# Kernel tuning notes

Hardware: AMD Instinct MI355X
Metric: run time of the kernel (lower is better)

Reference implementation:

```python
import jax, jax.numpy as jnp
import numpy as np

LMAX = 6
F_IN = 512      # sphere_fdim
F_HID = 8       # f_hidden
N_PTS = 192     # s2 healpix grid points (projector & feature-sphere kernel)
N_SO3GRID = 4000  # SO3Activation grid (resolution=10, ~20x10x20)
N_CONVGRID = 192  # so3_near_identity_grid (8 alpha x 3 beta x 8 gamma)
S2_DIM = (LMAX + 1) ** 2                            # 49
SO3_DIM = sum((2 * l + 1) ** 2 for l in range(LMAX + 1))  # 455
B = 128
C_ENC = 2048
H = W = 7


def setup_inputs() -> dict:
    key = jax.random.key(0)
    ks = jax.random.split(key, 11)
    return {
        "fmap": jax.random.normal(ks[0], (B, C_ENC, H, W), jnp.float32),
        "conv_w": jax.random.normal(ks[1], (F_IN, C_ENC), jnp.float32) / np.sqrt(C_ENC).astype(np.float32),
        "conv_b": jnp.zeros((F_IN,), jnp.float32),
        "proj_w": jax.random.uniform(ks[2], (H, W, N_PTS), jnp.float32) / (H * W),
        "proj_Y": jax.random.normal(ks[3], (N_PTS, S2_DIM), jnp.float32),
        "fs_w": jax.random.normal(ks[4], (F_IN, F_HID, N_PTS), jnp.float32),
        "fs_Y": jax.random.normal(ks[5], (N_PTS, S2_DIM), jnp.float32),
        "act_to": jax.random.normal(ks[6], (SO3_DIM, N_SO3GRID), jnp.float32) / np.sqrt(SO3_DIM).astype(np.float32),
        "act_from": jax.random.normal(ks[7], (N_SO3GRID, SO3_DIM), jnp.float32) / np.float32(N_SO3GRID),
        "so3_w": jax.random.normal(ks[8], (F_HID, 1, N_CONVGRID), jnp.float32),
        "so3_D": jax.random.normal(ks[9], (N_CONVGRID, SO3_DIM), jnp.float32),
    }


def _s2_to_so3_linear(x, psi, f_in):
    # e3nn o3.Linear(s2_irreps -> so3_irreps, internal_weights=False).
    # x: (B, f_in, S2_DIM) with per-l blocks of size 2l+1 (mul=1).
    # psi: (f_in, f_out, S2_DIM). Per l: outer product of input irrep with
    # weight irrep -> (2l+1)x(2l+1) Wigner block; path norm 1/sqrt(f_in*mul_in).
    outs = []
    for l in range(LMAX + 1):
        s, e = l * l, (l + 1) ** 2
        xl = x[:, :, s:e]          # (B, f_in, 2l+1)
        wl = psi[:, :, s:e]        # (f_in, f_out, 2l+1)
        ol = jnp.einsum('bfm,fgu->bgum', xl, wl) / np.sqrt(f_in).astype(np.float32)
        outs.append(ol.reshape(ol.shape[0], ol.shape[1], -1))
    return jnp.concatenate(outs, axis=-1)   # (B, f_out, SO3_DIM)


def _so3_to_so3_linear(x, psi, f_in):
    # e3nn o3.Linear(so3_irreps -> so3_irreps, internal_weights=False).
    # x: (B, f_in, SO3_DIM), per-l block (mul=2l+1, dim=2l+1) flattened [u, m].
    # psi: (f_in, f_out, SO3_DIM), per-l block (u_in, u_out).
    outs = []
    off = 0
    for l in range(LMAX + 1):
        d = 2 * l + 1
        xl = x[:, :, off:off + d * d].reshape(x.shape[0], f_in, d, d)
        wl = psi[:, :, off:off + d * d].reshape(f_in, psi.shape[1], d, d)
        ol = jnp.einsum('bfum,fguv->bgvm', xl, wl) / np.sqrt(f_in * d).astype(np.float32)
        outs.append(ol.reshape(ol.shape[0], ol.shape[1], -1))
        off += d * d
    return jnp.concatenate(outs, axis=-1)


def reference(fmap, conv_w, conv_b, proj_w, proj_Y, fs_w, fs_Y, act_to, act_from, so3_w, so3_D):
    # --- SpatialS2Projector: 1x1 conv, orthographic-grid weighting, S2 FT ---
    x = jnp.einsum('bchw,fc->bfhw', fmap, conv_w) + conv_b[None, :, None, None]
    x = jnp.einsum('bfhw,hwn->bfn', x, proj_w)                   # (B, 512, N_PTS)
    x = jnp.einsum('bfn,ni->bfi', x, proj_Y) / np.sqrt(N_PTS).astype(np.float32)  # (B, 512, 49)
    # --- feature sphere -> external weight for o3.Linear (S2 conv theorem) ---
    psi = jnp.einsum('fgn,ni->fgi', fs_w, fs_Y) / np.sqrt(N_PTS).astype(np.float32)  # (512, 8, 49)
    x = _s2_to_so3_linear(x, psi, F_IN)                          # (B, 8, 455)
    # --- SO3Activation: synthesize signal on SO3 grid, relu, analyze back ---
    g = jax.nn.relu(jnp.einsum('bfi,in->bfn', x, act_to))        # (B, 8, N_SO3GRID)
    x = jnp.einsum('bfn,ni->bfi', g, act_from)                   # (B, 8, 455)
    # --- SO3Convolution over near-identity grid ---
    psi2 = jnp.einsum('fgn,ni->fgi', so3_w, so3_D) / np.sqrt(N_CONVGRID).astype(np.float32)  # (8, 1, 455)
    x = _so3_to_so3_linear(x, psi2, F_HID)                       # (B, 1, 455)
    return x
```

## Files before the change

kernel.cpp:

```cpp
#include <hip/hip_runtime.h>
#include <hip/hip_bf16.h>

#define NB    128
#define CENC  2048
#define FIN   512
#define FHID  8
#define S2D   49
#define SO3D  455
#define HW    49

typedef unsigned short ushort_t;
typedef __bf16 bf16x8 __attribute__((ext_vector_type(8)));
typedef float  f32x4  __attribute__((ext_vector_type(4)));

#define GLD16(gp, lp) __builtin_amdgcn_global_load_lds( \
    (__attribute__((address_space(1))) const unsigned int*)(gp), \
    (__attribute__((address_space(3))) unsigned int*)(lp), 16, 0, 0)

__device__ __forceinline__ int soff(int l) { return l*(4*l*l-1)/3; }

__device__ __forceinline__ ushort_t f2bf(float x) {
  __hip_bfloat16 h = __float2bfloat16(x);
  return *reinterpret_cast<ushort_t*>(&h);
}
__device__ __forceinline__ float bf2f(ushort_t u) {
  __hip_bfloat16 h = *reinterpret_cast<__hip_bfloat16*>(&u);
  return __bfloat162float(h);
}


__device__ __forceinline__ void dev_gemm_nn(float* smem,
    const float* __restrict__ A, const float* __restrict__ B, float* __restrict__ C,
    int M, int N, int K, int lda, int ldb, int ldc, float alpha, int bx, int by,
    int cmode, ushort_t* __restrict__ psiTout)
{
  float* As = smem;
  float* Bs = smem + 32*68;
  const int tid = threadIdx.x;
  const int tx = tid & 15, ty = tid >> 4;
  const int n0 = bx * 64, m0 = by * 64;
  float acc[4][4] = {};
  for (int k0 = 0; k0 < K; k0 += 32) {
    {
      const int kk = tid & 31, mmB = tid >> 5;
      #pragma unroll
      for (int j = 0; j < 8; ++j) {
        const int mm = mmB + 8*j;
        const int m = m0 + mm, k = k0 + kk;
        As[kk*68 + mm] = (m < M && k < K) ? A[(size_t)m*lda + k] : 0.f;
      }
    }
    {
      const int nn = tid & 63, kkB = tid >> 6;
      #pragma unroll
      for (int j = 0; j < 8; ++j) {
        const int kk = kkB + 4*j;
        const int n = n0 + nn, k = k0 + kk;
        Bs[kk*68 + nn] = (n < N && k < K) ? B[(size_t)k*ldb + n] : 0.f;
      }
    }
    __syncthreads();
    #pragma unroll
    for (int kk = 0; kk < 32; ++kk) {
      const float4 a4 = *(const float4*)&As[kk*68 + ty*4];
      const float4 b4 = *(const float4*)&Bs[kk*68 + tx*4];
      const float av[4] = {a4.x,a4.y,a4.z,a4.w};
      const float bv[4] = {b4.x,b4.y,b4.z,b4.w};
      #pragma unroll
      for (int i = 0; i < 4; ++i)
        #pragma unroll
        for (int j = 0; j < 4; ++j)
          acc[i][j] = fmaf(av[i], bv[j], acc[i][j]);
    }
    __syncthreads();
  }
  if (cmode == 1) {
    #pragma unroll
    for (int i = 0; i < 4; ++i) {
      const int m = m0 + ty*4 + i;
      const int f = m >> 3, g = m & 7;
      #pragma unroll
      for (int j = 0; j < 4; ++j) {
        const int n = tx*4 + j;
        psiTout[(size_t)(g*64 + n)*512 + f] = (n < 49) ? f2bf(acc[i][j]*alpha) : (ushort_t)0;
      }
    }
    return;
  }
  #pragma unroll
  for (int i = 0; i < 4; ++i) {
    const int m = m0 + ty*4 + i;
    if (m >= M) continue;
    #pragma unroll
    for (int j = 0; j < 4; ++j) {
      const int n = n0 + tx*4 + j;
      if (n >= N) continue;
      C[(size_t)m*ldc + n] = acc[i][j] * alpha;
    }
  }
}

__device__ __forceinline__ void dev_transpose_cvt64(float* smem,
    const float* __restrict__ in, int R, int C,
    ushort_t* __restrict__ out, int Rp, int Cp, int bx, int by)
{
  float (*t)[65] = (float(*)[65])smem;
  const int c0 = bx*64, r0 = by*64;
  const int tid = threadIdx.x;
  const int cl = tid & 63, rlB = tid >> 6;
  #pragma unroll
  for (int p = 0; p < 16; ++p) {
    const int rl = rlB + p*4;
    const int r = r0 + rl, c = c0 + cl;
    t[rl][cl] = (r < R && c < C) ? in[(size_t)r*C + c] : 0.f;
  }
  __syncthreads();
  #pragma unroll
  for (int p = 0; p < 4; ++p) {
    const int c = p*16 + (tid >> 4);
    const int r4 = (tid & 15) * 4;
    unsigned int lo = (unsigned int)f2bf(t[r4+0][c]) | ((unsigned int)f2bf(t[r4+1][c]) << 16);
    unsigned int hi = (unsigned int)f2bf(t[r4+2][c]) | ((unsigned int)f2bf(t[r4+3][c]) << 16);
    *(uint2*)&out[(size_t)(c0 + c)*Rp + r0 + r4] = make_uint2(lo, hi);
  }
}

__device__ __forceinline__ void dev_transpose_fmap(float* smem,
    const float* __restrict__ fmap, ushort_t* __restrict__ out, int cc, int b)
{
  float* Fs = smem;
  const int tid = threadIdx.x;
  const int c0 = cc*64;
  const float* fsrc = fmap + ((size_t)b*CENC + c0)*HW;
  for (int idx = tid; idx < 784; idx += 256)
    *(float4*)&Fs[idx*4] = *(const float4*)&fsrc[idx*4];
  __syncthreads();
  for (int idx = tid; idx < 784; idx += 256) {
    const int h = idx >> 4, c4 = (idx & 15) * 4;
    unsigned int lo = (unsigned int)f2bf(Fs[(c4+0)*49 + h]) | ((unsigned int)f2bf(Fs[(c4+1)*49 + h]) << 16);
    unsigned int hi = (unsigned int)f2bf(Fs[(c4+2)*49 + h]) | ((unsigned int)f2bf(Fs[(c4+3)*49 + h]) << 16);
    *(uint2*)&out[(size_t)(b*49 + h)*CENC + c0 + c4] = make_uint2(lo, hi);
  }
}

__device__ __forceinline__ void dev_sumP(float* smem,
    const float* __restrict__ proj_w, const float* __restrict__ proj_Y,
    float* __restrict__ sumP)
{
  float* colsum = smem;
  const int tid = threadIdx.x;
  if (tid < 192) {
    float s = 0.f;
    for (int h = 0; h < 49; ++h) s += proj_w[h*192 + tid];
    colsum[tid] = s;
  }
  __syncthreads();
  if (tid < 64) {
    float s = 0.f;
    if (tid < 49) for (int k = 0; k < 192; ++k) s += colsum[k] * proj_Y[k*49 + tid];
    sumP[tid] = (tid < 49) ? s * 0.07216878364870323f : 0.f;
  }
}

__global__ __launch_bounds__(256) void prep_all(
    const float* __restrict__ fmap, const float* __restrict__ conv_w,
    const float* __restrict__ proj_w, const float* __restrict__ proj_Y,
    const float* __restrict__ fs_w, const float* __restrict__ fs_Y,
    const float* __restrict__ act_to, const float* __restrict__ act_from,
    const float* __restrict__ so3_w, const float* __restrict__ so3_D,
    float* __restrict__ wP, float* __restrict__ wSumP, float* __restrict__ wPsi2,
    ushort_t* __restrict__ psiT,
    ushort_t* __restrict__ actToT, ushort_t* __restrict__ actFromT,
    ushort_t* __restrict__ cwT, ushort_t* __restrict__ fmapT)
{
  __shared__ float smem[4352];
  const int blk = blockIdx.x;
  const float is192 = 0.07216878364870323f;
  if (blk < 1) {
    dev_gemm_nn(smem, proj_w, proj_Y, wP, 49,49,192, 192,49,49, is192, 0, 0, 0, nullptr);
  } else if (blk < 9) {
    dev_gemm_nn(smem, so3_w, so3_D, wPsi2, 8,455,192, 192,455,455, is192, blk-1, 0, 0, nullptr);
  } else if (blk < 73) {
    dev_gemm_nn(smem, fs_w, fs_Y, nullptr, 4096,49,192, 192,49,0, is192, 0, blk-9, 1, psiT);
  } else if (blk < 585) {
    const int t = blk-73;   dev_transpose_cvt64(smem, act_to, 455, 4000, actToT, 512, 4096, t & 63, t >> 6);
  } else if (blk < 1097) {
    const int t = blk-585;  dev_transpose_cvt64(smem, act_from, 4000, 455, actFromT, 4096, 512, t & 7, t >> 3);
  } else if (blk < 1353) {
    const int t = blk-1097; dev_transpose_cvt64(smem, conv_w, 512, 2048, cwT, 512, 2048, t & 31, t >> 5);
  } else if (blk < 5449) {
    const int t = blk-1353; dev_transpose_fmap(smem, fmap, fmapT, t & 31, t >> 5);
  } else {
    dev_sumP(smem, proj_w, proj_Y, wSumP);
  }
}

__global__ __launch_bounds__(256) void gemm_w2t(
    const ushort_t* __restrict__ A, const ushort_t* __restrict__ B,
    const float* __restrict__ conv_b,
    ushort_t* __restrict__ Cb, float* __restrict__ bpsi)
{
  __shared__ ushort_t Alds[64*64];
  __shared__ ushort_t Blds[128*64];
  __shared__ float bred[256];
  const int tid = threadIdx.x;
  const int wv = tid >> 6, ln = tid & 63;
  const int col = ln & 15, quad = ln >> 4;
  const int m0 = blockIdx.y * 64, n0 = blockIdx.x * 128;
  const int lda = 512, ldb = 512, ldc = 2048, K = 512;
  const bool doB = (blockIdx.x == 0);
  const int br = tid & 63, bp = tid >> 6;

  const int rl = ln >> 3;
  const int gsw = (ln & 7) ^ rl;
  const ushort_t* aP[2]; const ushort_t* bP[4];
  ushort_t* aL[2]; ushort_t* bL[4];
  #pragma unroll
  for (int r = 0; r < 2; ++r) {
    const int R = wv*16 + r*8;
    aP[r] = A + (size_t)(m0 + R + rl)*lda + gsw*8;
    aL[r] = &Alds[R*64];
  }
  #pragma unroll
  for (int r = 0; r < 4; ++r) {
    const int R = wv*32 + r*8;
    bP[r] = B + (size_t)(n0 + R + rl)*ldb + gsw*8;
    bL[r] = &Blds[R*64];
  }

  f32x4 acc[4][2];
  #pragma unroll
  for (int i = 0; i < 4; ++i)
    #pragma unroll
    for (int j = 0; j < 2; ++j)
      acc[i][j] = (f32x4){0.f,0.f,0.f,0.f};
  float bacc = 0.f;

  for (int k0 = 0; k0 < K; k0 += 64) {
    #pragma unroll
    for (int r = 0; r < 2; ++r) { GLD16(aP[r], aL[r]); aP[r] += 64; }
    #pragma unroll
    for (int r = 0; r < 4; ++r) { GLD16(bP[r], bL[r]); bP[r] += 64; }
    __syncthreads();
    #pragma unroll
    for (int ks = 0; ks < 2; ++ks) {
      bf16x8 af[4], bfr[2];
      #pragma unroll
      for (int i = 0; i < 4; ++i) {
        const int row = i*16 + col;
        af[i] = *(bf16x8*)&Alds[row*64 + (((ks*4 + quad) ^ (row & 7)) << 3)];
      }
      #pragma unroll
      for (int j = 0; j < 2; ++j) {
        const int row = wv*32 + j*16 + col;
        bfr[j] = *(bf16x8*)&Blds[row*64 + (((ks*4 + quad) ^ (row & 7)) << 3)];
      }
      #pragma unroll
      for (int i = 0; i < 4; ++i)
        #pragma unroll
        for (int j = 0; j < 2; ++j)
          acc[i][j] = __builtin_amdgcn_mfma_f32_16x16x32_bf16(af[i], bfr[j], acc[i][j], 0, 0, 0);
    }
    if (doB) {
      #pragma unroll
      for (int qq = 0; qq < 2; ++qq) {
        const int q = bp*2 + qq;
        const int lo = (q ^ (br & 7)) << 3;
        #pragma unroll
        for (int e = 0; e < 8; ++e)
          bacc = fmaf(conv_b[k0 + q*8 + e], bf2f(Alds[br*64 + lo + e]), bacc);
      }
    }
    __syncthreads();
  }

  #pragma unroll
  for (int i = 0; i < 4; ++i) {
    const int mBase = m0 + i*16 + quad*4;
    #pragma unroll
    for (int j = 0; j < 2; ++j) {
      const int n = n0 + wv*32 + j*16 + col;
      #pragma unroll
      for (int r = 0; r < 4; ++r)
        Cb[(size_t)(mBase+r)*ldc + n] = f2bf(acc[i][j][r]);
    }
  }
  if (doB) {
    bred[bp*64 + br] = bacc;
    __syncthreads();
    if (tid < 64)
      bpsi[m0 + tid] = bred[tid] + bred[64+tid] + bred[128+tid] + bred[192+tid];
  }
}

__global__ __launch_bounds__(512) void gemm8w_nt(
    const ushort_t* __restrict__ A, const ushort_t* __restrict__ B, void* __restrict__ Cv,
    int M, int N, int K, int lda, int ldb, int ldc,
    int mode, int kPartLen)
{
  __shared__ ushort_t Alds[128*64];
  __shared__ ushort_t Blds[128*64];
  const int tid = threadIdx.x;
  const int wv = tid >> 6, ln = tid & 63;
  const int col = ln & 15, quad = ln >> 4;
  const int wr = wv >> 2, wc = wv & 3;
  const int m0 = blockIdx.y * 128, n0 = blockIdx.x * 128;
  int kStart = 0, kEnd = K;
  float*    C  = (float*)Cv;
  ushort_t* Cb = (ushort_t*)Cv;
  if (mode == 2) {
    kStart = blockIdx.z * kPartLen;
    kEnd = min(K, kStart + kPartLen);
    C += (size_t)blockIdx.z * (size_t)M * (size_t)ldc;
  }

  const int rl = ln >> 3;
  const int gsw = (ln & 7) ^ rl;
  const ushort_t* aP[2]; const ushort_t* bP[2];
  ushort_t* aL[2]; ushort_t* bL[2];
  #pragma unroll
  for (int r = 0; r < 2; ++r) {
    const int R = wv*16 + r*8;
    aP[r] = A + (size_t)(m0 + R + rl)*lda + kStart + gsw*8;
    aL[r] = &Alds[R*64];
    bP[r] = B + (size_t)(n0 + R + rl)*ldb + kStart + gsw*8;
    bL[r] = &Blds[R*64];
  }

  f32x4 acc[4][2];
  #pragma unroll
  for (int i = 0; i < 4; ++i)
    #pragma unroll
    for (int j = 0; j < 2; ++j)
      acc[i][j] = (f32x4){0.f,0.f,0.f,0.f};

  for (int k0 = kStart; k0 < kEnd; k0 += 64) {
    #pragma unroll
    for (int r = 0; r < 2; ++r) { GLD16(aP[r], aL[r]); aP[r] += 64; }
    #pragma unroll
    for (int r = 0; r < 2; ++r) { GLD16(bP[r], bL[r]); bP[r] += 64; }
    __syncthreads();
    #pragma unroll
    for (int ks = 0; ks < 2; ++ks) {
      bf16x8 af[4], bfr[2];
      #pragma unroll
      for (int i = 0; i < 4; ++i) {
        const int row = wr*64 + i*16 + col;
        af[i] = *(bf16x8*)&Alds[row*64 + (((ks*4 + quad) ^ (row & 7)) << 3)];
      }
      #pragma unroll
      for (int j = 0; j < 2; ++j) {
        const int row = wc*32 + j*16 + col;
        bfr[j] = *(bf16x8*)&Blds[row*64 + (((ks*4 + quad) ^ (row & 7)) << 3)];
      }
      #pragma unroll
      for (int i = 0; i < 4; ++i)
        #pragma unroll
        for (int j = 0; j < 2; ++j)
          acc[i][j] = __builtin_amdgcn_mfma_f32_16x16x32_bf16(af[i], bfr[j], acc[i][j], 0, 0, 0);
    }
    __syncthreads();
  }

  #pragma unroll
  for (int i = 0; i < 4; ++i) {
    const int mBase = m0 + wr*64 + i*16 + quad*4;
    #pragma unroll
    for (int j = 0; j < 2; ++j) {
      const int n = n0 + wc*32 + j*16 + col;
      if (mode == 1) {
        #pragma unroll
        for (int r = 0; r < 4; ++r)
          Cb[(size_t)(mBase+r)*ldc + n] = f2bf(fmaxf(acc[i][j][r], 0.f));
      } else {
        #pragma unroll
        for (int r = 0; r < 4; ++r)
          C[(size_t)(mBase+r)*ldc + n] = acc[i][j][r];
      }
    }
  }
}

__global__ __launch_bounds__(256) void gather_y(
    const float* __restrict__ T, const float* __restrict__ P,
    const float* __restrict__ sumP, const float* __restrict__ bpsi,
    ushort_t* __restrict__ y)
{
  __shared__ float Tg[49*64];
  __shared__ float Pl[49*49];
  __shared__ float sPl[49];
  __shared__ float bps[64];
  const int tid = threadIdx.x;
  const int g = blockIdx.x & 7, b = blockIdx.x >> 3;
  for (int idx = tid; idx < 49*64; idx += 256) {
    const int h = idx >> 6, c = idx & 63;
    Tg[idx] = T[(size_t)(b*49 + h)*512 + g*64 + c];
  }
  for (int idx = tid; idx < 2401; idx += 256) Pl[idx] = P[idx];
  if (tid < 49) sPl[tid] = sumP[tid];
  if (tid < 64) bps[tid] = bpsi[g*64 + tid];
  __syncthreads();
  #pragma unroll
  for (int rr = 0; rr < 2; ++rr) {
    const int j = tid + rr*256;
    float v = 0.f;
    if (j < SO3D) {
      int l;
      if (j < 1) l = 0; else if (j < 10) l = 1; else if (j < 35) l = 2;
      else if (j < 84) l = 3; else if (j < 165) l = 4; else if (j < 286) l = 5; else l = 6;
      const int so = soff(l), d = 2*l+1;
      const int r = j - so;
      const int u = r / d, m = r - u*d;
      const int i = l*l + m, colT = l*l + u;
      float acc = 0.f;
      #pragma unroll 7
      for (int h = 0; h < 49; ++h)
        acc = fmaf(Pl[h*49 + i], Tg[h*64 + colT], acc);
      v = (acc + sPl[i]*bps[colT]) * 0.044194173824159216f;
    }
    y[(size_t)(b*8+g)*512 + j] = f2bf(v);
  }
}

__global__ __launch_bounds__(512) void so3_final(
    const float* __restrict__ zpart, const float* __restrict__ psi2,
    float* __restrict__ out)
{
  __shared__ float Zs[8*SO3D];
  __shared__ float P2s[8*SO3D];
  const int b = blockIdx.x, tid = threadIdx.x;
  for (int idx = tid; idx < 8*SO3D; idx += 512) {
    const int f = idx / SO3D, i = idx - f*SO3D;
    float s = 0.f;
    #pragma unroll
    for (int p = 0; p < 8; ++p)
      s += zpart[((size_t)p*1024 + (size_t)b*FHID + f)*512 + i];
    Zs[idx] = s;
    P2s[idx] = psi2[idx];
  }
  __syncthreads();
  if (tid < SO3D) {
    const int i = tid;
    int l;
    if (i < 1) l = 0; else if (i < 10) l = 1; else if (i < 35) l = 2;
    else if (i < 84) l = 3; else if (i < 165) l = 4; else if (i < 286) l = 5; else l = 6;
    const int so = soff(l), d = 2*l+1;
    const int r = i - so;
    const int v = r / d, m = r - v*d;
    float acc = 0.f;
    for (int f = 0; f < 8; ++f)
      for (int u = 0; u < d; ++u)
        acc = fmaf(Zs[f*SO3D + so + u*d + m], P2s[f*SO3D + so + u*d + v], acc);
    const float scale = rsqrtf(8.0f * (float)d);
    out[(size_t)b*SO3D + i] = acc * scale;
  }
}

extern "C" void kernel_launch(void* const* d_in, const int* in_sizes, int n_in,
                              void* d_out, int out_size, void* d_ws, size_t ws_size,
                              hipStream_t stream) {
  const float* fmap    = (const float*)d_in[0];
  const float* conv_w  = (const float*)d_in[1];
  const float* conv_b  = (const float*)d_in[2];
  const float* proj_w  = (const float*)d_in[3];
  const float* proj_Y  = (const float*)d_in[4];
  const float* fs_w    = (const float*)d_in[5];
  const float* fs_Y    = (const float*)d_in[6];
  const float* act_to  = (const float*)d_in[7];
  const float* act_from= (const float*)d_in[8];
  const float* so3_w   = (const float*)d_in[9];
  const float* so3_D   = (const float*)d_in[10];
  float* out           = (float*)d_out;

  char* wsb = (char*)d_ws;
  float*    wP       = (float*)(wsb + 0);
  float*    wSumP    = (float*)(wsb + 9728);
  float*    wPsi2    = (float*)(wsb + 9984);
  ushort_t* actToT   = (ushort_t*)(wsb + 24576);
  ushort_t* actFromT = (ushort_t*)(wsb + 4218880);
  ushort_t* yPad     = (ushort_t*)(wsb + 8413184);
  ushort_t* psiT     = (ushort_t*)(wsb + 9461760);
  float*    bpsi     = (float*)(wsb + 9986048);
  ushort_t* W2T      = (ushort_t*)(wsb + 9988096);
  ushort_t* fmapT    = (ushort_t*)(wsb + 12085248);
  ushort_t* cwT      = (ushort_t*)(wsb + 39872512);
  float*    Tbuf     = (float*)(wsb + 41969664);
  ushort_t* gBuf     = (ushort_t*)(wsb + 12085248);
  float*    zPart    = (float*)(wsb + 20473856);

  prep_all<<<dim3(5450), 256, 0, stream>>>(
      fmap, conv_w, proj_w, proj_Y, fs_w, fs_Y, act_to, act_from, so3_w, so3_D,
      wP, wSumP, wPsi2, psiT, actToT, actFromT, cwT, fmapT);
  gemm_w2t<<<dim3(16,8), 256, 0, stream>>>(psiT, cwT, conv_b, W2T, bpsi);
  gemm8w_nt<<<dim3(4,49), 512, 0, stream>>>(fmapT, W2T, Tbuf,
      6272, 512, 2048, 2048, 2048, 512, 0, 0);
  gather_y<<<dim3(1024), 256, 0, stream>>>(Tbuf, wP, wSumP, bpsi, yPad);
  gemm8w_nt<<<dim3(32,8), 512, 0, stream>>>(yPad, actToT, gBuf,
      1024, 4096, 512, 512, 512, 4096, 1, 0);
  gemm8w_nt<<<dim3(4,8,8), 512, 0, stream>>>(gBuf, actFromT, zPart,
      1024, 512, 4096, 4096, 4096, 512, 2, 512);
  so3_final<<<dim3(128), 512, 0, stream>>>(zPart, wPsi2, out);
}
```

Baseline: 229.9 us.

## Reorder contractions: project fmap over spatial grid first, then per-l block-diagonal GEMM

Replaces the fmap transpose plus the big 6272x512x2048 conv GEMM and the gather step with two new kernels. One applies the 49x49 projection matrix to each fmap tile via MFMA, producing a bf16 (B*64)x2048 intermediate. The other performs per-degree block-diagonal GEMMs against W2T to form y directly. The aim is to cut the dominant conv GEMM work and the fp32 intermediate traffic. In exchange it adds another bf16 rounding of the projected activations and uses small, unevenly sized tiles in the block-diagonal kernel (172 blocks, each with a K=2048 loop).

```diff
diff --git a/kernel.cpp b/kernel.cpp
--- a/kernel.cpp
+++ b/kernel.cpp
@@ -125,24 +125,6 @@
   }
 }
 
-__device__ __forceinline__ void dev_transpose_fmap(float* smem,
-    const float* __restrict__ fmap, ushort_t* __restrict__ out, int cc, int b)
-{
-  float* Fs = smem;
-  const int tid = threadIdx.x;
-  const int c0 = cc*64;
-  const float* fsrc = fmap + ((size_t)b*CENC + c0)*HW;
-  for (int idx = tid; idx < 784; idx += 256)
-    *(float4*)&Fs[idx*4] = *(const float4*)&fsrc[idx*4];
-  __syncthreads();
-  for (int idx = tid; idx < 784; idx += 256) {
-    const int h = idx >> 4, c4 = (idx & 15) * 4;
-    unsigned int lo = (unsigned int)f2bf(Fs[(c4+0)*49 + h]) | ((unsigned int)f2bf(Fs[(c4+1)*49 + h]) << 16);
-    unsigned int hi = (unsigned int)f2bf(Fs[(c4+2)*49 + h]) | ((unsigned int)f2bf(Fs[(c4+3)*49 + h]) << 16);
-    *(uint2*)&out[(size_t)(b*49 + h)*CENC + c0 + c4] = make_uint2(lo, hi);
-  }
-}
-
 __device__ __forceinline__ void dev_sumP(float* smem,
     const float* __restrict__ proj_w, const float* __restrict__ proj_Y,
     float* __restrict__ sumP)
@@ -163,7 +145,7 @@
 }
 
 __global__ __launch_bounds__(256) void prep_all(
-    const float* __restrict__ fmap, const float* __restrict__ conv_w,
+    const float* __restrict__ conv_w,
     const float* __restrict__ proj_w, const float* __restrict__ proj_Y,
     const float* __restrict__ fs_w, const float* __restrict__ fs_Y,
     const float* __restrict__ act_to, const float* __restrict__ act_from,
@@ -171,7 +153,7 @@
     float* __restrict__ wP, float* __restrict__ wSumP, float* __restrict__ wPsi2,
     ushort_t* __restrict__ psiT,
     ushort_t* __restrict__ actToT, ushort_t* __restrict__ actFromT,
-    ushort_t* __restrict__ cwT, ushort_t* __restrict__ fmapT)
+    ushort_t* __restrict__ cwT)
 {
   __shared__ float smem[4352];
   const int blk = blockIdx.x;
@@ -188,10 +170,88 @@
     const int t = blk-585;  dev_transpose_cvt64(smem, act_from, 4000, 455, actFromT, 4096, 512, t & 7, t >> 3);
   } else if (blk < 1353) {
     const int t = blk-1097; dev_transpose_cvt64(smem, conv_w, 512, 2048, cwT, 512, 2048, t & 31, t >> 5);
-  } else if (blk < 5449) {
-    const int t = blk-1353; dev_transpose_fmap(smem, fmap, fmapT, t & 31, t >> 5);
   } else {
     dev_sumP(smem, proj_w, proj_Y, wSumP);
+  }
+}
+
+__global__ __launch_bounds__(256) void xpt_gemm(
+    const float* __restrict__ fmap, const float* __restrict__ wP,
+    ushort_t* __restrict__ xPT)
+{
+  __shared__ ushort_t Wl[64*64];
+  __shared__ ushort_t Fl[128*64];
+  const int tid = threadIdx.x;
+  const int b = blockIdx.x >> 4, ct = blockIdx.x & 15;
+  const int c0 = ct*128;
+  for (int idx = tid; idx < 4096; idx += 256) {
+    const int i = idx >> 6, hw = idx & 63;
+    const float v = (i < 49 && hw < 49) ? wP[hw*49 + i] : 0.f;
+    const int pos = i*64 + ((((hw>>3) ^ (i & 7)) << 3) | (hw & 7));
+    Wl[pos] = f2bf(v);
+  }
+  const float* src = fmap + ((size_t)b*CENC + c0)*HW;
+  #pragma unroll
+  for (int q = 0; q < 7; ++q) {
+    const int f4 = q*256 + tid;
+    if (f4 < 1568) {
+      const float4 v = *(const float4*)&src[f4*4];
+      const float vv[4] = {v.x,v.y,v.z,v.w};
+      const int e0 = f4*4;
+      #pragma unroll
+      for (int t = 0; t < 4; ++t) {
+        const int e = e0 + t;
+        const int r = e/49, hw = e - r*49;
+        const int pos = r*64 + ((((hw>>3) ^ (r & 7)) << 3) | (hw & 7));
+        Fl[pos] = f2bf(vv[t]);
+      }
+    }
+  }
+  for (int idx = tid; idx < 128*15; idx += 256) {
+    const int r = idx/15, hw = 49 + (idx - (idx/15)*15);
+    const int pos = r*64 + ((((hw>>3) ^ (r & 7)) << 3) | (hw & 7));
+    Fl[pos] = 0;
+  }
+  __syncthreads();
+
+  const int wv = tid >> 6, ln = tid & 63;
+  const int col = ln & 15, quad = ln >> 4;
+  f32x4 acc[4][2];
+  #pragma unroll
+  for (int i = 0; i < 4; ++i)
+    #pragma unroll
+    for (int j = 0; j < 2; ++j)
+      acc[i][j] = (f32x4){0.f,0.f,0.f,0.f};
+  #pragma unroll
+  for (int ks = 0; ks < 2; ++ks) {
+    bf16x8 af[4], bfr[2];
+    #pragma unroll
+    for (int i = 0; i < 4; ++i) {
+      const int row = i*16 + col;
+      af[i] = *(bf16x8*)&Wl[row*64 + (((ks*4 + quad) ^ (row & 7)) << 3)];
+    }
+    #pragma unroll
+    for (int j = 0; j < 2; ++j) {
+      const int row = wv*32 + j*16 + col;
+      bfr[j] = *(bf16x8*)&Fl[row*64 + (((ks*4 + quad) ^ (row & 7)) << 3)];
+    }
+    #pragma unroll
+    for (int i = 0; i < 4; ++i)
+      #pragma unroll
+      for (int j = 0; j < 2; ++j)
+        acc[i][j] = __builtin_amdgcn_mfma_f32_16x16x32_bf16(af[i], bfr[j], acc[i][j], 0, 0, 0);
+  }
+  #pragma unroll
+  for (int i = 0; i < 4; ++i) {
+    #pragma unroll
+    for (int j = 0; j < 2; ++j) {
+      #pragma unroll
+      for (int r = 0; r < 4; ++r) {
+        const int irow = i*16 + quad*4 + r;
+        const int c = c0 + wv*32 + j*16 + col;
+        xPT[(size_t)(b*64 + irow)*2048 + c] = f2bf(acc[i][j][r]);
+      }
+    }
   }
 }
 
@@ -290,6 +350,113 @@
     __syncthreads();
     if (tid < 64)
       bpsi[m0 + tid] = bred[tid] + bred[64+tid] + bred[128+tid] + bred[192+tid];
+  }
+}
+
+__global__ __launch_bounds__(256) void y_blockdiag(
+    const ushort_t* __restrict__ xPT, const ushort_t* __restrict__ W2T,
+    const float* __restrict__ sumP, const float* __restrict__ bpsi,
+    ushort_t* __restrict__ y)
+{
+  const int blk = blockIdx.x, tid = threadIdx.x;
+  if (blk >= 164) {
+    const int bz = blk - 164;
+    for (int idx = tid; idx < 7296; idx += 256) {
+      const int row = bz*128 + idx/57, cp = 455 + (idx - (idx/57)*57);
+      y[(size_t)row*512 + cp] = 0;
+    }
+    return;
+  }
+  __shared__ ushort_t Asl[64*64];
+  __shared__ ushort_t Bsl[64*64];
+  int l, lstart;
+  if      (blk < 2)   { l=0; lstart=0; }
+  else if (blk < 8)   { l=1; lstart=2; }
+  else if (blk < 18)  { l=2; lstart=8; }
+  else if (blk < 32)  { l=3; lstart=18; }
+  else if (blk < 68)  { l=4; lstart=32; }
+  else if (blk < 112) { l=5; lstart=68; }
+  else                { l=6; lstart=112; }
+  const int d = 2*l+1, ll = l*l, Ml = 8*d;
+  const int local = blk - lstart, ntc = 2*d;
+  const int mt = local / ntc, nt = local - mt*ntc;
+  const int m0 = mt*64, n0 = nt*64;
+
+  const int wv = tid >> 6, ln = tid & 63;
+  const int col = ln & 15, quad = ln >> 4;
+  const int wr = wv >> 1, wc = wv & 1;
+  const int rl = ln >> 3;
+  const int gsw = (ln & 7) ^ rl;
+
+  const ushort_t* aP[2]; const ushort_t* bP[2];
+  ushort_t* aL[2]; ushort_t* bL[2];
+  #pragma unroll
+  for (int r = 0; r < 2; ++r) {
+    const int R = wv*16 + r*8;
+    const int mu = m0 + R + rl;
+    int grow;
+    if (mu < Ml) { const int g = mu/d, u = mu - g*d; grow = g*64 + ll + u; }
+    else grow = 511;
+    aP[r] = W2T + (size_t)grow*2048 + gsw*8;
+    aL[r] = &Asl[R*64];
+    const int nu = n0 + R + rl;
+    const int bb = nu/d, m = nu - bb*d;
+    bP[r] = xPT + (size_t)(bb*64 + ll + m)*2048 + gsw*8;
+    bL[r] = &Bsl[R*64];
+  }
+
+  f32x4 acc[2][2];
+  #pragma unroll
+  for (int i = 0; i < 2; ++i)
+    #pragma unroll
+    for (int j = 0; j < 2; ++j)
+      acc[i][j] = (f32x4){0.f,0.f,0.f,0.f};
+
+  for (int k0 = 0; k0 < 2048; k0 += 64) {
+    #pragma unroll
+    for (int r = 0; r < 2; ++r) { GLD16(aP[r], aL[r]); aP[r] += 64; }
+    #pragma unroll
+    for (int r = 0; r < 2; ++r) { GLD16(bP[r], bL[r]); bP[r] += 64; }
+    __syncthreads();
+    #pragma unroll
+    for (int ks = 0; ks < 2; ++ks) {
+      bf16x8 af[2], bfr[2];
+      #pragma unroll
+      for (int i = 0; i < 2; ++i) {
+        const int row = wr*32 + i*16 + col;
+        af[i] = *(bf16x8*)&Asl[row*64 + (((ks*4 + quad) ^ (row & 7)) << 3)];
+      }
+      #pragma unroll
+      for (int j = 0; j < 2; ++j) {
+        const int row = wc*32 + j*16 + col;
+        bfr[j] = *(bf16x8*)&Bsl[row*64 + (((ks*4 + quad) ^ (row & 7)) << 3)];
+      }
+      #pragma unroll
+      for (int i = 0; i < 2; ++i)
+        #pragma unroll
+        for (int j = 0; j < 2; ++j)
+          acc[i][j] = __builtin_amdgcn_mfma_f32_16x16x32_bf16(af[i], bfr[j], acc[i][j], 0, 0, 0);
+    }
+    __syncthreads();
+  }
+
+  const float isq512 = 0.044194173824159216f;
+  const int sol = soff(l);
+  #pragma unroll
+  for (int i = 0; i < 2; ++i) {
+    #pragma unroll
+    for (int j = 0; j < 2; ++j) {
+      #pragma unroll
+      for (int r = 0; r < 4; ++r) {
+        const int mu = m0 + wr*32 + i*16 + quad*4 + r;
+        if (mu >= Ml) continue;
+        const int nu = n0 + wc*32 + j*16 + col;
+        const int g = mu/d, u = mu - g*d;
+        const int bb = nu/d, m = nu - bb*d;
+        const float v = (acc[i][j][r] + sumP[ll+m]*bpsi[g*64 + ll + u]) * isq512;
+        y[(size_t)(bb*8 + g)*512 + sol + u*d + m] = f2bf(v);
+      }
+    }
   }
 }
 
@@ -378,47 +545,6 @@
           C[(size_t)(mBase+r)*ldc + n] = acc[i][j][r];
       }
     }
-  }
-}
-
-__global__ __launch_bounds__(256) void gather_y(
-    const float* __restrict__ T, const float* __restrict__ P,
-    const float* __restrict__ sumP, const float* __restrict__ bpsi,
-    ushort_t* __restrict__ y)
-{
-  __shared__ float Tg[49*64];
-  __shared__ float Pl[49*49];
-  __shared__ float sPl[49];
-  __shared__ float bps[64];
-  const int tid = threadIdx.x;
-  const int g = blockIdx.x & 7, b = blockIdx.x >> 3;
-  for (int idx = tid; idx < 49*64; idx += 256) {
-    const int h = idx >> 6, c = idx & 63;
-    Tg[idx] = T[(size_t)(b*49 + h)*512 + g*64 + c];
-  }
-  for (int idx = tid; idx < 2401; idx += 256) Pl[idx] = P[idx];
-  if (tid < 49) sPl[tid] = sumP[tid];
-  if (tid < 64) bps[tid] = bpsi[g*64 + tid];
-  __syncthreads();
-  #pragma unroll
-  for (int rr = 0; rr < 2; ++rr) {
-    const int j = tid + rr*256;
-    float v = 0.f;
-    if (j < SO3D) {
-      int l;
-      if (j < 1) l = 0; else if (j < 10) l = 1; else if (j < 35) l = 2;
-      else if (j < 84) l = 3; else if (j < 165) l = 4; else if (j < 286) l = 5; else l = 6;
-      const int so = soff(l), d = 2*l+1;
-      const int r = j - so;
-      const int u = r / d, m = r - u*d;
-      const int i = l*l + m, colT = l*l + u;
-      float acc = 0.f;
-      #pragma unroll 7
-      for (int h = 0; h < 49; ++h)
-        acc = fmaf(Pl[h*49 + i], Tg[h*64 + colT], acc);
-      v = (acc + sPl[i]*bps[colT]) * 0.044194173824159216f;
-    }
-    y[(size_t)(b*8+g)*512 + j] = f2bf(v);
   }
 }
 
@@ -482,19 +608,17 @@
   ushort_t* psiT     = (ushort_t*)(wsb + 9461760);
   float*    bpsi     = (float*)(wsb + 9986048);
   ushort_t* W2T      = (ushort_t*)(wsb + 9988096);
-  ushort_t* fmapT    = (ushort_t*)(wsb + 12085248);
-  ushort_t* cwT      = (ushort_t*)(wsb + 39872512);
-  float*    Tbuf     = (float*)(wsb + 41969664);
+  ushort_t* xPT      = (ushort_t*)(wsb + 12085248);
+  ushort_t* cwT      = (ushort_t*)(wsb + 45639680);
   ushort_t* gBuf     = (ushort_t*)(wsb + 12085248);
   float*    zPart    = (float*)(wsb + 20473856);
 
-  prep_all<<<dim3(5450), 256, 0, stream>>>(
-      fmap, conv_w, proj_w, proj_Y, fs_w, fs_Y, act_to, act_from, so3_w, so3_D,
-      wP, wSumP, wPsi2, psiT, actToT, actFromT, cwT, fmapT);
+  prep_all<<<dim3(1354), 256, 0, stream>>>(
+      conv_w, proj_w, proj_Y, fs_w, fs_Y, act_to, act_from, so3_w, so3_D,
+      wP, wSumP, wPsi2, psiT, actToT, actFromT, cwT);
+  xpt_gemm<<<dim3(2048), 256, 0, stream>>>(fmap, wP, xPT);
   gemm_w2t<<<dim3(16,8), 256, 0, stream>>>(psiT, cwT, conv_b, W2T, bpsi);
-  gemm8w_nt<<<dim3(4,49), 512, 0, stream>>>(fmapT, W2T, Tbuf,
-      6272, 512, 2048, 2048, 2048, 512, 0, 0);
-  gather_y<<<dim3(1024), 256, 0, stream>>>(Tbuf, wP, wSumP, bpsi, yPad);
+  y_blockdiag<<<dim3(172), 256, 0, stream>>>(xPT, W2T, wSumP, bpsi, yPad);
   gemm8w_nt<<<dim3(32,8), 512, 0, stream>>>(yPad, actToT, gBuf,
       1024, 4096, 512, 512, 512, 4096, 1, 0);
   gemm8w_nt<<<dim3(4,8,8), 512, 0, stream>>>(gBuf, actFromT, zPart,
```

New measurement: 222.9 us. 1.03x faster.
